# Optimization experiments

Hardware: AMD Instinct MI355X
Metric: run time of the kernel (lower is better)

The kernel has to match this reference:

```python
import jax, jax.numpy as jnp
import numpy as np
from jax import lax

B, C, W = 16, 64, 125000  # batch, EEG channels, raw samples
KH, KW, SW, OC = 3, 2500, 1250, 32


def setup_inputs() -> dict:
    key = jax.random.key(0)
    ks = jax.random.split(key, 10)
    inp = {
        "x": jax.random.normal(ks[0], (B, 1, C, W), dtype=jnp.float32),
        # Conv2d(1->32, kernel=(3,2500))
        "conv_w": jax.random.normal(ks[1], (OC, 1, KH, KW), dtype=jnp.float32) * 0.02,
        "conv_b": jax.random.normal(ks[2], (OC,), dtype=jnp.float32) * 0.02,
        # Conv2d(32->1, kernel=(1,1))
        "conv2_w": jax.random.normal(ks[3], (1, OC, 1, 1), dtype=jnp.float32) * 0.1,
        "conv2_b": jax.random.normal(ks[4], (1,), dtype=jnp.float32) * 0.1,
        # nn.RNN(input_size=1, hidden_size=1): scalar weights
        "w_ih": jax.random.normal(ks[5], (1, 1), dtype=jnp.float32),
        "w_hh": jax.random.normal(ks[6], (1, 1), dtype=jnp.float32),
        "b_ih": jax.random.normal(ks[7], (1,), dtype=jnp.float32) * 0.1,
        "b_hh": jax.random.normal(ks[8], (1,), dtype=jnp.float32) * 0.1,
        # torch.rand(num_layers=1, B, 1) hidden init, reused for every row i
        "h0": jax.random.uniform(ks[9], (1, B, 1), dtype=jnp.float32),
    }
    return inp


def reference(x, conv_w, conv_b, conv2_w, conv2_b, w_ih, w_hh, b_ih, b_hh, h0):
    # F.pad(x, (0,0,1,1), 'replicate'): pad channel (height) dim by 1 each side
    xp = jnp.pad(x, ((0, 0), (0, 0), (1, 1), (0, 0)), mode="edge")
    # conv + relu -> [B, 32, C, T]
    y = lax.conv_general_dilated(
        xp, conv_w, window_strides=(1, SW), padding="VALID",
        dimension_numbers=("NCHW", "OIHW", "NCHW"))
    y = jax.nn.relu(y + conv_b[None, :, None, None])
    # 1x1 conv 32->1 + relu -> [B, C, T]
    z = jnp.einsum("bohw,o->bhw", y, conv2_w[0, :, 0, 0]) + conv2_b[0]
    z = jax.nn.relu(z)
    # Elman RNN with scalar weights, scanned over T; carry is [B, C]
    wih, whh = w_ih[0, 0], w_hh[0, 0]
    bias = b_ih[0] + b_hh[0]
    h_init = jnp.broadcast_to(h0[0, :, 0][:, None], z.shape[:2])  # [B, C]

    def step(h, xt):  # xt: [B, C]
        h = jnp.tanh(wih * xt + whh * h + bias)
        return h, None

    xs = jnp.moveaxis(z, -1, 0)  # [T, B, C]
    h_final, _ = lax.scan(step, h_init, xs)
    return jax.nn.sigmoid(h_final)  # [B, C]
```

## Files before the change

kernel.cpp:

```cpp
#include <hip/hip_runtime.h>
#include <math.h>

#define B_ 16
#define C_ 64
#define T_ 99
#define KW_ 1250
#define KP_ 1280
#define N_ 192
#define M_ (B_*C_*100)
#define BM 128
#define BK 32
#define NSC 10
#define ASTRIDE 136

typedef __attribute__((ext_vector_type(8))) _Float16 half8;
typedef __attribute__((ext_vector_type(2))) _Float16 half2_t;
typedef __attribute__((ext_vector_type(4))) float f32x4;
typedef __attribute__((ext_vector_type(2), aligned(8))) float f32x2;

__global__ __launch_bounds__(256) void wconv_kernel(const float* __restrict__ cw,
                                                    _Float16* __restrict__ wh)
{
    int n = blockIdx.x;
    int o = n / 6, rem = n - o * 6, kh = rem >> 1, hf = rem & 1;
    const float* src = cw + o * 7500 + kh * 2500 + hf * 1250;
    for (int k = threadIdx.x; k < KP_; k += 256)
        wh[n * KP_ + k] = (k < KW_) ? (_Float16)src[k] : (_Float16)0.f;
}

__global__ __launch_bounds__(256, 2) void gemm_kernel(const float* __restrict__ x,
                                                      const _Float16* __restrict__ wh,
                                                      _Float16* __restrict__ P)
{
    __shared__ __align__(16) _Float16 smA[BM * ASTRIDE];

    const int tid  = threadIdx.x;
    const int bt   = blockIdx.x;
    const int lane = tid & 63;
    const int wave = tid >> 6;
    const int wm   = (wave & 1) * 64;
    const int wn   = (wave >> 1) * 96;
    const int l15  = lane & 15;
    const int lq   = lane >> 4;

    const int h   = tid >> 5;
    const int lw  = tid & 31;
    const int lw2 = lw * 2;
    const int rbase = h * 16;
    const float* apx = x + (size_t)(bt * BM + rbase) * KW_ + lw2;

    const _Float16* bbase = wh + (size_t)(wn + l15) * KP_ + lq * 8;

    f32x4 acc[4][6];
#pragma unroll
    for (int mi = 0; mi < 4; mi++)
#pragma unroll
        for (int ni = 0; ni < 6; ni++) acc[mi][ni] = (f32x4){0.f, 0.f, 0.f, 0.f};

    f32x2 areg[16][2];

#define LOADA(sc_) do {                                                          \
        const float* p_ = apx + (sc_) * 128;                                     \
        if ((sc_) < NSC - 1) {                                                   \
            _Pragma("unroll") for (int i = 0; i < 16; i++)                       \
            _Pragma("unroll") for (int w = 0; w < 2; w++)                        \
                areg[i][w] = *(const f32x2*)(p_ + (size_t)i * KW_ + w * 64);     \
        } else {                                                                 \
            _Pragma("unroll") for (int i = 0; i < 16; i++)                       \
            _Pragma("unroll") for (int w = 0; w < 2; w++) {                      \
                int k_ = (NSC - 1) * 128 + w * 64 + lw2;                         \
                areg[i][w] = (k_ <= KW_ - 2)                                     \
                    ? *(const f32x2*)(p_ + (size_t)i * KW_ + w * 64)             \
                    : (f32x2){0.f, 0.f};                                         \
            }                                                                    \
        }                                                                        \
    } while (0)

    LOADA(0);

    for (int sc = 0; sc < NSC; sc++) {
#pragma unroll
        for (int i = 0; i < 16; i++) {
            const int r = rbase + i;
#pragma unroll
            for (int w = 0; w < 2; w++) {
                half2_t hh = {(_Float16)areg[i][w].x, (_Float16)areg[i][w].y};
                *(half2_t*)(smA + r * ASTRIDE + w * 64 + lw2) = hh;
            }
        }

        half8 bfr[6];
#pragma unroll
        for (int ni = 0; ni < 6; ni++)
            bfr[ni] = *(const half8*)(bbase + (size_t)ni * 16 * KP_
                                            + (size_t)(sc * 4) * BK);

        asm volatile("s_waitcnt lgkmcnt(0)" ::: "memory");
        __builtin_amdgcn_s_barrier();
        __builtin_amdgcn_sched_barrier(0);

        if (sc + 1 < NSC) LOADA(sc + 1);

#pragma unroll
        for (int ckl = 0; ckl < 4; ckl++) {
            if (ckl > 0) {
#pragma unroll
                for (int ni = 0; ni < 6; ni++)
                    bfr[ni] = *(const half8*)(bbase + (size_t)ni * 16 * KP_
                                                    + (size_t)(sc * 4 + ckl) * BK);
            }
            half8 afr[4];
#pragma unroll
            for (int mi = 0; mi < 4; mi++)
                afr[mi] = *(const half8*)(smA + (wm + mi * 16 + l15) * ASTRIDE
                                              + ckl * 32 + lq * 8);
#pragma unroll
            for (int mi = 0; mi < 4; mi++)
#pragma unroll
                for (int ni = 0; ni < 6; ni++)
                    acc[mi][ni] = __builtin_amdgcn_mfma_f32_16x16x32_f16(
                        afr[mi], bfr[ni], acc[mi][ni], 0, 0, 0);
        }

        asm volatile("s_waitcnt lgkmcnt(0)" ::: "memory");
        __builtin_amdgcn_s_barrier();
        __builtin_amdgcn_sched_barrier(0);
    }
#undef LOADA

#pragma unroll
    for (int mi = 0; mi < 4; mi++) {
#pragma unroll
        for (int r2 = 0; r2 < 4; r2++) {
            int rloc = wm + mi * 16 + lq * 4 + r2;
            int xr   = bt * BM + rloc;
            int bc   = xr / 100;
            int j    = xr - bc * 100;
            size_t mp = ((size_t)(bc >> 6) * 100 + j) * 64 + (bc & 63);
#pragma unroll
            for (int ni = 0; ni < 6; ni++) {
                int n = wn + ni * 16 + l15;
                P[mp * N_ + n] = (_Float16)acc[mi][ni][r2];
            }
        }
    }
}

__global__ __launch_bounds__(256) void combine_kernel(const _Float16* __restrict__ P,
                                                      const float* __restrict__ conv_b,
                                                      const float* __restrict__ c2w,
                                                      const float* __restrict__ c2b,
                                                      float* __restrict__ z)
{
    __shared__ float Pl[64][193];
    __shared__ float red[4][64];
    const int t   = blockIdx.x;
    const int b   = blockIdx.y;
    const int tid = threadIdx.x;
    const int c   = tid & 63;
    const int og  = tid >> 6;

    float v[8];
#pragma unroll
    for (int o = 0; o < 8; o++) v[o] = conv_b[og * 8 + o];

    for (int hf = 0; hf < 2; hf++) {
        const int j = t + hf;
        const _Float16* Pb = P + (size_t)((b * 100 + j) * 64) * N_;
        __syncthreads();
#pragma unroll
        for (int i = 0; i < 6; i++) {
            int e   = i * 256 + tid;
            half8 hdat = *(const half8*)(Pb + e * 8);
            int row = e / 24;
            int col = (e - row * 24) * 8;
#pragma unroll
            for (int u = 0; u < 8; u++) Pl[row][col + u] = (float)hdat[u];
        }
        __syncthreads();
#pragma unroll
        for (int kh = 0; kh < 3; kh++) {
            int r = c + kh - 1;
            r = r < 0 ? 0 : (r > 63 ? 63 : r);
#pragma unroll
            for (int o = 0; o < 8; o++)
                v[o] += Pl[r][(og * 8 + o) * 6 + kh * 2 + hf];
        }
    }

    float part = 0.f;
#pragma unroll
    for (int o = 0; o < 8; o++) part += fmaxf(v[o], 0.f) * c2w[og * 8 + o];
    red[og][c] = part;
    __syncthreads();
    if (og == 0) {
        float zz = red[0][c] + red[1][c] + red[2][c] + red[3][c] + c2b[0];
        z[t * (B_ * C_) + b * 64 + c] = fmaxf(zz, 0.f);
    }
}

__global__ __launch_bounds__(256) void rnn_kernel(const float* __restrict__ z,
                                                  const float* __restrict__ w_ih,
                                                  const float* __restrict__ w_hh,
                                                  const float* __restrict__ b_ih,
                                                  const float* __restrict__ b_hh,
                                                  const float* __restrict__ h0,
                                                  float* __restrict__ out)
{
    __shared__ float zs[50][256];
    const int tid = threadIdx.x;
    const int g   = blockIdx.x * 256 + tid;
    const int b   = g >> 6;
    const float wih  = w_ih[0];
    const float whh  = w_hh[0];
    const float bias = b_ih[0] + b_hh[0];
    float h = h0[b];
    for (int t0 = 0; t0 < T_; t0 += 50) {
        const int nt = (T_ - t0) < 50 ? (T_ - t0) : 50;
        __syncthreads();
        for (int tt = 0; tt < nt; tt++)
            zs[tt][tid] = z[(t0 + tt) * (B_ * C_) + g];
        __syncthreads();
        for (int tt = 0; tt < nt; tt++)
            h = tanhf(fmaf(wih, zs[tt][tid], fmaf(whh, h, bias)));
    }
    out[g] = 1.f / (1.f + expf(-h));
}

extern "C" void kernel_launch(void* const* d_in, const int* in_sizes, int n_in,
                              void* d_out, int out_size, void* d_ws, size_t ws_size,
                              hipStream_t stream)
{
    const float* x   = (const float*)d_in[0];
    const float* cw  = (const float*)d_in[1];
    const float* cb  = (const float*)d_in[2];
    const float* c2w = (const float*)d_in[3];
    const float* c2b = (const float*)d_in[4];
    const float* wih = (const float*)d_in[5];
    const float* whh = (const float*)d_in[6];
    const float* bih = (const float*)d_in[7];
    const float* bhh = (const float*)d_in[8];
    const float* h0  = (const float*)d_in[9];
    float* out = (float*)d_out;

    const size_t whbytes = (size_t)N_ * KP_ * sizeof(_Float16);
    const size_t pbytes  = (size_t)M_ * N_ * sizeof(_Float16);
    const size_t zbytes  = (size_t)B_ * C_ * T_ * sizeof(float);

    if (ws_size < whbytes + pbytes + zbytes) return;

    _Float16* wh = (_Float16*)d_ws;
    _Float16* P  = (_Float16*)((char*)d_ws + whbytes);
    float*    z  = (float*)((char*)d_ws + whbytes + pbytes);

    wconv_kernel<<<N_, 256, 0, stream>>>(cw, wh);
    gemm_kernel<<<M_ / BM, 256, 0, stream>>>(x, wh, P);
    combine_kernel<<<dim3(T_, B_), 256, 0, stream>>>(P, cb, c2w, c2b, z);
    rnn_kernel<<<4, 256, 0, stream>>>(z, wih, whh, bih, bhh, h0, out);
}
```

Measured before the change: 787.7 us.

## Shrink GEMM tile to 32 rows and stage whole K slice in swizzled LDS

The GEMM block tile shrinks from 128 to 32 rows. Each block loads its full 32x1280 half-precision A slice into shared memory once, using an XOR swizzle to avoid bank conflicts, then runs the whole K loop with no per-chunk barriers or register double-buffering. Each wave now covers 48 output columns with a smaller accumulator set. This gives four times as many blocks and removes the per-chunk synchronisation. The cost is more redundant weight (B) reads from global memory per block, since weight reuse drops with the smaller M tile, and no overlap between the A-load phase and compute within a block.

```diff
diff --git a/kernel.cpp b/kernel.cpp
--- a/kernel.cpp
+++ b/kernel.cpp
@@ -8,10 +8,8 @@
 #define KP_ 1280
 #define N_ 192
 #define M_ (B_*C_*100)
-#define BM 128
-#define BK 32
-#define NSC 10
-#define ASTRIDE 136
+#define BM 32
+#define NCHUNK 40
 
 typedef __attribute__((ext_vector_type(8))) _Float16 half8;
 typedef __attribute__((ext_vector_type(2))) _Float16 half2_t;
@@ -32,113 +30,79 @@
                                                       const _Float16* __restrict__ wh,
                                                       _Float16* __restrict__ P)
 {
-    __shared__ __align__(16) _Float16 smA[BM * ASTRIDE];
+    __shared__ __align__(16) _Float16 smA[BM * KP_];
 
     const int tid  = threadIdx.x;
     const int bt   = blockIdx.x;
     const int lane = tid & 63;
     const int wave = tid >> 6;
-    const int wm   = (wave & 1) * 64;
-    const int wn   = (wave >> 1) * 96;
+    const int wn   = wave * 48;
     const int l15  = lane & 15;
     const int lq   = lane >> 4;
-
-    const int h   = tid >> 5;
-    const int lw  = tid & 31;
-    const int lw2 = lw * 2;
-    const int rbase = h * 16;
-    const float* apx = x + (size_t)(bt * BM + rbase) * KW_ + lw2;
+    const int l4   = lane >> 2;
+    const int lm4  = lane & 3;
+
+    {
+        const float* xb = x + (size_t)(bt * BM + wave * 8) * KW_;
+#pragma unroll
+        for (int rr = 0; rr < 8; rr++) {
+            const int row = wave * 8 + rr;
+            const float* xr = xb + (size_t)rr * KW_;
+            _Float16* drow = smA + row * KP_;
+            const int r7 = row & 7;
+#pragma unroll
+            for (int s = 0; s < 10; s++) {
+                int c = s * 128 + lane * 2;
+                f32x2 v = (c <= KW_ - 2) ? *(const f32x2*)(xr + c)
+                                         : (f32x2){0.f, 0.f};
+                int blk = (s * 16 + l4) ^ r7;
+                *(half2_t*)(drow + blk * 8 + lm4 * 2) =
+                    (half2_t){(_Float16)v.x, (_Float16)v.y};
+            }
+        }
+    }
+    __syncthreads();
 
     const _Float16* bbase = wh + (size_t)(wn + l15) * KP_ + lq * 8;
 
-    f32x4 acc[4][6];
-#pragma unroll
-    for (int mi = 0; mi < 4; mi++)
-#pragma unroll
-        for (int ni = 0; ni < 6; ni++) acc[mi][ni] = (f32x4){0.f, 0.f, 0.f, 0.f};
-
-    f32x2 areg[16][2];
-
-#define LOADA(sc_) do {                                                          \
-        const float* p_ = apx + (sc_) * 128;                                     \
-        if ((sc_) < NSC - 1) {                                                   \
-            _Pragma("unroll") for (int i = 0; i < 16; i++)                       \
-            _Pragma("unroll") for (int w = 0; w < 2; w++)                        \
-                areg[i][w] = *(const f32x2*)(p_ + (size_t)i * KW_ + w * 64);     \
-        } else {                                                                 \
-            _Pragma("unroll") for (int i = 0; i < 16; i++)                       \
-            _Pragma("unroll") for (int w = 0; w < 2; w++) {                      \
-                int k_ = (NSC - 1) * 128 + w * 64 + lw2;                         \
-                areg[i][w] = (k_ <= KW_ - 2)                                     \
-                    ? *(const f32x2*)(p_ + (size_t)i * KW_ + w * 64)             \
-                    : (f32x2){0.f, 0.f};                                         \
-            }                                                                    \
-        }                                                                        \
-    } while (0)
-
-    LOADA(0);
-
-    for (int sc = 0; sc < NSC; sc++) {
-#pragma unroll
-        for (int i = 0; i < 16; i++) {
-            const int r = rbase + i;
-#pragma unroll
-            for (int w = 0; w < 2; w++) {
-                half2_t hh = {(_Float16)areg[i][w].x, (_Float16)areg[i][w].y};
-                *(half2_t*)(smA + r * ASTRIDE + w * 64 + lw2) = hh;
-            }
-        }
-
-        half8 bfr[6];
-#pragma unroll
-        for (int ni = 0; ni < 6; ni++)
-            bfr[ni] = *(const half8*)(bbase + (size_t)ni * 16 * KP_
-                                            + (size_t)(sc * 4) * BK);
-
-        asm volatile("s_waitcnt lgkmcnt(0)" ::: "memory");
-        __builtin_amdgcn_s_barrier();
-        __builtin_amdgcn_sched_barrier(0);
-
-        if (sc + 1 < NSC) LOADA(sc + 1);
-
-#pragma unroll
-        for (int ckl = 0; ckl < 4; ckl++) {
-            if (ckl > 0) {
-#pragma unroll
-                for (int ni = 0; ni < 6; ni++)
-                    bfr[ni] = *(const half8*)(bbase + (size_t)ni * 16 * KP_
-                                                    + (size_t)(sc * 4 + ckl) * BK);
-            }
-            half8 afr[4];
-#pragma unroll
-            for (int mi = 0; mi < 4; mi++)
-                afr[mi] = *(const half8*)(smA + (wm + mi * 16 + l15) * ASTRIDE
-                                              + ckl * 32 + lq * 8);
-#pragma unroll
-            for (int mi = 0; mi < 4; mi++)
-#pragma unroll
-                for (int ni = 0; ni < 6; ni++)
-                    acc[mi][ni] = __builtin_amdgcn_mfma_f32_16x16x32_f16(
-                        afr[mi], bfr[ni], acc[mi][ni], 0, 0, 0);
-        }
-
-        asm volatile("s_waitcnt lgkmcnt(0)" ::: "memory");
-        __builtin_amdgcn_s_barrier();
-        __builtin_amdgcn_sched_barrier(0);
-    }
-#undef LOADA
-
-#pragma unroll
-    for (int mi = 0; mi < 4; mi++) {
+    f32x4 acc[2][3];
+#pragma unroll
+    for (int mi = 0; mi < 2; mi++)
+#pragma unroll
+        for (int ni = 0; ni < 3; ni++) acc[mi][ni] = (f32x4){0.f, 0.f, 0.f, 0.f};
+
+#pragma unroll 4
+    for (int ck = 0; ck < NCHUNK; ck++) {
+        half8 bfr[3];
+#pragma unroll
+        for (int ni = 0; ni < 3; ni++)
+            bfr[ni] = *(const half8*)(bbase + (size_t)ni * 16 * KP_ + ck * 32);
+        half8 afr[2];
+#pragma unroll
+        for (int mi = 0; mi < 2; mi++) {
+            int row = mi * 16 + l15;
+            int blk = (ck * 4 + lq) ^ (row & 7);
+            afr[mi] = *(const half8*)(smA + row * KP_ + blk * 8);
+        }
+#pragma unroll
+        for (int mi = 0; mi < 2; mi++)
+#pragma unroll
+            for (int ni = 0; ni < 3; ni++)
+                acc[mi][ni] = __builtin_amdgcn_mfma_f32_16x16x32_f16(
+                    afr[mi], bfr[ni], acc[mi][ni], 0, 0, 0);
+    }
+
+#pragma unroll
+    for (int mi = 0; mi < 2; mi++) {
 #pragma unroll
         for (int r2 = 0; r2 < 4; r2++) {
-            int rloc = wm + mi * 16 + lq * 4 + r2;
+            int rloc = mi * 16 + lq * 4 + r2;
             int xr   = bt * BM + rloc;
             int bc   = xr / 100;
             int j    = xr - bc * 100;
             size_t mp = ((size_t)(bc >> 6) * 100 + j) * 64 + (bc & 63);
 #pragma unroll
-            for (int ni = 0; ni < 6; ni++) {
+            for (int ni = 0; ni < 3; ni++) {
                 int n = wn + ni * 16 + l15;
                 P[mp * N_ + n] = (_Float16)acc[mi][ni][r2];
             }
```

Result: slower. 874.9 us (+11.1%).
